# Optimization experiments

Hardware: AMD Instinct MI355X
Metric: run time of the kernel (lower is better)

Reference implementation:

```python
import jax, jax.numpy as jnp
import numpy as np

VOX_X, VOX_Y, VOX_Z = 256, 256, 20   # ceil((pc_range[3:]-pc_range[:3]) / 0.4)
OUT_H, OUT_W, OUT_Z = 200, 200, 16   # hard-coded F.interpolate target in forward
C = 80                               # out_channels; sparse feat dim must match for concat
N_PTS = 200000
BS = 1
EPS = 1e-5


def _lin_interp(x, axis, out_size):
    """1D linear interp along `axis`, matching torch align_corners=False."""
    in_size = x.shape[axis]
    pos = (jnp.arange(out_size, dtype=jnp.float32) + 0.5) * (in_size / out_size) - 0.5
    pos = jnp.clip(pos, 0.0, in_size - 1)
    i0 = jnp.floor(pos).astype(jnp.int32)
    i1 = jnp.minimum(i0 + 1, in_size - 1)
    w = pos - i0.astype(jnp.float32)
    x0 = jnp.take(x, i0, axis=axis)
    x1 = jnp.take(x, i1, axis=axis)
    wshape = [1] * x.ndim
    wshape[axis] = out_size
    w = w.reshape(wshape)
    return x0 * (1.0 - w) + x1 * w


def setup_inputs() -> dict:
    key = jax.random.key(0)
    ks = jax.random.split(key, 8)
    bev_feats = jax.random.normal(ks[0], (BS, C, OUT_H, OUT_W, OUT_Z), dtype=jnp.float32)
    # coords: [batch_idx, x, y, z] with per-column valid ranges
    cb = jax.random.randint(ks[1], (N_PTS, 1), 0, BS, dtype=jnp.int32)
    cx = jax.random.randint(ks[2], (N_PTS, 1), 0, VOX_X, dtype=jnp.int32)
    cy = jax.random.randint(ks[3], (N_PTS, 1), 0, VOX_Y, dtype=jnp.int32)
    cz = jax.random.randint(ks[4], (N_PTS, 1), 0, VOX_Z, dtype=jnp.int32)
    coords = jnp.concatenate([cb, cx, cy, cz], axis=1)
    feats = jax.random.normal(ks[5], (N_PTS, C), dtype=jnp.float32)
    w_conv = jax.random.normal(ks[6], (C, 2 * C), dtype=jnp.float32) * (1.0 / np.sqrt(2 * C))
    b_conv = jnp.zeros((C,), dtype=jnp.float32)
    return {
        "bev_feats": bev_feats, "coords": coords, "feats": feats,
        "w_conv": w_conv, "b_conv": b_conv,
        "bn_gamma": jnp.ones((C,), jnp.float32), "bn_beta": jnp.zeros((C,), jnp.float32),
        "bn_mean": jnp.zeros((C,), jnp.float32), "bn_var": jnp.ones((C,), jnp.float32),
    }


def reference(bev_feats, coords, feats, w_conv, b_conv, bn_gamma, bn_beta, bn_mean, bn_var):
    bs = bev_feats.shape[0]
    voxel = jnp.zeros((bs, VOX_X, VOX_Y, VOX_Z, C), dtype=jnp.float32)
    voxel = voxel.at[coords[:, 0], coords[:, 1], coords[:, 2], coords[:, 3]].set(feats)
    # permute(0,4,2,1,3): (bs, X, Y, Z, C) -> (bs, C, Y, X, Z)
    prior = jnp.transpose(voxel, (0, 4, 2, 1, 3))
    # trilinear interpolate (256,256,20) -> (200,200,16), align_corners=False (separable)
    prior = _lin_interp(prior, 2, OUT_H)
    prior = _lin_interp(prior, 3, OUT_W)
    prior = _lin_interp(prior, 4, OUT_Z)
    # concat on channels -> 1x1x1 conv3d -> BN (eval stats) -> residual -> ReLU
    x = jnp.concatenate([bev_feats, prior], axis=1)  # (bs, 2C, H, W, Z)
    y = jnp.einsum('bchwz,oc->bohwz', x, w_conv) + b_conv[None, :, None, None, None]
    inv = bn_gamma * jax.lax.rsqrt(bn_var + EPS)
    y = y * inv[None, :, None, None, None] + (bn_beta - bn_mean * inv)[None, :, None, None, None]
    return jax.nn.relu(y + bev_feats)
```

## Files before the change

### kernel.cpp

```cpp
#include <hip/hip_runtime.h>
#include <hip/hip_bf16.h>

#define VXX 256
#define VYY 256
#define VZZ 20
#define NC  80
#define OH  200
#define OW  200
#define OZ  16
#define SPATIAL (OH*OW*OZ)
#define NVOX (VXX*VYY*VZZ)
#define EPSV 1e-5f
#define NS 64
#define RS 168
#define NWG (SPATIAL/NS)
#define X_FOOT 6
#define NCELL (2*X_FOOT*VZZ)
#define SLOTS 48
#define STR32 41

typedef float  f32x4 __attribute__((ext_vector_type(4)));
typedef short  s16x8 __attribute__((ext_vector_type(8)));

__device__ __forceinline__ ushort f2bf(float f) {
    uint u = __builtin_bit_cast(uint, f);
    u += 0x7FFFu + ((u >> 16) & 1u);
    return (ushort)(u >> 16);
}

__global__ void init_winner_k(int* __restrict__ w) {
    int i = blockIdx.x * 256 + threadIdx.x;
    if (i < NVOX) w[i] = -1;
}

__global__ void scatter_k(const int* __restrict__ coords, int npts,
                          int* __restrict__ winner) {
    int i = blockIdx.x * 256 + threadIdx.x;
    if (i >= npts) return;
    int b = coords[i*4+0];
    int x = coords[i*4+1];
    int y = coords[i*4+2];
    int z = coords[i*4+3];
    int vi = ((b*VXX + x)*VYY + y)*VZZ + z;
    atomicMax(&winner[vi], i);
}

__global__ void prep_k(const float* __restrict__ wconv,
                       const float* __restrict__ bconv,
                       const float* __restrict__ gamma,
                       const float* __restrict__ beta,
                       const float* __restrict__ mean,
                       const float* __restrict__ var,
                       ushort* __restrict__ wfrag,
                       float2* __restrict__ bnss) {
    int tid = threadIdx.x;
    for (int idx = tid; idx < 25*512; idx += 256) {
        int f   = idx >> 9;
        int rem = idx & 511;
        int l   = rem >> 3;
        int j   = rem & 7;
        int mt  = f / 5;
        int ks  = f - mt*5;
        int o   = mt*16 + (l & 15);
        int c   = ks*32 + (l >> 4)*8 + j;
        wfrag[idx] = f2bf(wconv[o*160 + c]);
    }
    if (tid < NC) {
        float inv = gamma[tid] * rsqrtf(var[tid] + EPSV);
        bnss[tid] = make_float2(inv, bconv[tid]*inv + beta[tid] - mean[tid]*inv);
    }
}

__launch_bounds__(256, 5)
__global__ void fused_k(const float* __restrict__ bev,
                        const float* __restrict__ feats,
                        const int*  __restrict__ winner,
                        const ushort* __restrict__ wfrag,
                        const float2* __restrict__ bnss,
                        float* __restrict__ out) {
    __shared__ __align__(16) ushort x_lds[NS * RS];
    __shared__ uint   rows_lds[SLOTS*STR32];
    __shared__ int    idx_lds[NCELL];
    __shared__ int    slot_pi[SLOTS];
    __shared__ int    wavecnt[4];

    const int tid   = threadIdx.x;
    const int bid   = blockIdx.x;
    const int swzb  = (bid & 7) * (NWG/8) + (bid >> 3);
    const int sbase = swzb * NS;
    const int sl    = tid & 63;
    const int quarter = tid >> 6;
    const int wv    = tid >> 6, lane = tid & 63;

    const int h  = sbase / (OW * OZ);
    const int w0 = (sbase >> 4) % OW;
    float posy = (h + 0.5f) * ((float)VYY/(float)OH) - 0.5f;
    posy = fminf(fmaxf(posy, 0.f), (float)(VYY-1));
    const int   y0 = (int)posy;
    const int   y1 = min(y0+1, VYY-1);
    const float fy = posy - (float)y0;
    float posx0 = (w0 + 0.5f) * ((float)VXX/(float)OW) - 0.5f;
    posx0 = fminf(fmaxf(posx0, 0.f), (float)(VXX-1));
    const int xmin = (int)posx0;

    float4 bv[5];
    {
        const int q16 = lane & 15, mm = lane >> 4;
        #pragma unroll
        for (int it = 0; it < 5; ++it) {
            int cbase = (it*4 + wv) * 4;
            bv[it] = *(const float4*)&bev[(cbase+mm)*SPATIAL + sbase + q16*4];
        }
    }

    int pi = -1;
    if (tid < NCELL) {
        int fz  = tid % VZZ;
        int fx  = (tid / VZZ) % X_FOOT;
        int fyc = tid / (VZZ * X_FOOT);
        int xx  = min(xmin + fx, VXX-1);
        int yy  = fyc ? y1 : y0;
        pi = winner[(xx*VYY + yy)*VZZ + fz];
    }
    unsigned long long bm = __ballot(pi >= 0);
    if (lane == 0) wavecnt[wv] = __popcll(bm);
    __syncthreads();
    int base = 0, nstot = 0;
    #pragma unroll
    for (int w2 = 0; w2 < 4; ++w2) {
        int c2 = wavecnt[w2];
        if (w2 < wv) base += c2;
        nstot += c2;
    }
    if (tid < NCELL) {
        int v = -1;
        if (pi >= 0) {
            int slot = base + __popcll(bm & ((1ull << lane) - 1ull));
            if (slot < SLOTS) { slot_pi[slot] = pi; v = slot; }
            else v = -(pi + 2);
        }
        idx_lds[tid] = v;
    }
    __syncthreads();
    const int nst = min(nstot, SLOTS);

    const float4* feats4 = (const float4*)feats;
    const int myslot = tid >> 2, part = tid & 3;
    const bool rowact = (myslot < nst);
    float4 rbuf[5];
    if (rowact) {
        const float4* p = feats4 + slot_pi[myslot]*20 + part*5;
        #pragma unroll
        for (int q = 0; q < 5; ++q) rbuf[q] = p[q];
    }

    {
        const int q16 = lane & 15, mm = lane >> 4;
        #pragma unroll
        for (int it = 0; it < 5; ++it) {
            int cbase = (it*4 + wv) * 4;
            const float4 v = bv[it];
            uint u0 = (uint)f2bf(v.x) | ((uint)f2bf(v.y) << 16);
            uint u1 = (uint)f2bf(v.z) | ((uint)f2bf(v.w) << 16);
            uint us[4];
            #pragma unroll
            for (int j = 0; j < 4; ++j) {
                int src = q16 + 16*j;
                uint t0 = (uint)__shfl((int)u0, src, 64);
                uint t1 = (uint)__shfl((int)u1, src, 64);
                uint sel = (mm & 2) ? t1 : t0;
                us[j] = (mm & 1) ? (sel >> 16) : (sel & 0xffffu);
            }
            uint2 o2 = make_uint2(us[0] | (us[1] << 16), us[2] | (us[3] << 16));
            int row = q16*4 + mm;
            *(uint2*)&x_lds[row*RS + cbase] = o2;
        }
    }

    if (rowact) {
        uint* dst = &rows_lds[myslot*STR32 + part*10];
        #pragma unroll
        for (int q = 0; q < 5; ++q) {
            dst[2*q]   = (uint)f2bf(rbuf[q].x) | ((uint)f2bf(rbuf[q].y) << 16);
            dst[2*q+1] = (uint)f2bf(rbuf[q].z) | ((uint)f2bf(rbuf[q].w) << 16);
        }
    }
    __syncthreads();

    {
        const int z = sl & 15;
        const int w = w0 + (sl >> 4);
        float posx = (w + 0.5f) * ((float)VXX/(float)OW) - 0.5f;
        posx = fminf(fmaxf(posx, 0.f), (float)(VXX-1));
        int x0 = (int)posx; int x1 = min(x0+1, VXX-1);
        float fxw = posx - (float)x0;
        float posz = (z + 0.5f) * ((float)VZZ/(float)OZ) - 0.5f;
        posz = fminf(fmaxf(posz, 0.f), (float)(VZZ-1));
        int z0 = (int)posz; int z1 = min(z0+1, VZZ-1);
        float fzw = posz - (float)z0;
        const int fx0 = x0 - xmin, fx1 = x1 - xmin;

        float acc20[20];
        #pragma unroll
        for (int j = 0; j < 20; ++j) acc20[j] = 0.f;

        #pragma unroll
        for (int k = 0; k < 8; ++k) {
            int kz = k & 1, kx = (k>>1)&1, ky = k>>2;
            int cell = (ky*X_FOOT + (kx ? fx1 : fx0))*VZZ + (kz ? z1 : z0);
            int v = idx_lds[cell];
            if (v == -1) continue;
            float wtk = (ky?fy:1.f-fy) * (kx?fxw:1.f-fxw) * (kz?fzw:1.f-fzw);
            if (v >= 0) {
                const uint* r = &rows_lds[v*STR32 + quarter*10];
                #pragma unroll
                for (int qq = 0; qq < 10; ++qq) {
                    uint u = r[qq];
                    float lo = __builtin_bit_cast(float, u << 16);
                    float hi = __builtin_bit_cast(float, u & 0xffff0000u);
                    acc20[2*qq]   += wtk * lo;
                    acc20[2*qq+1] += wtk * hi;
                }
            } else {
                const float4* p = feats4 + (-v - 2)*20 + quarter*5;
                #pragma unroll
                for (int q = 0; q < 5; ++q) {
                    float4 f = p[q];
                    acc20[4*q]   += wtk*f.x; acc20[4*q+1] += wtk*f.y;
                    acc20[4*q+2] += wtk*f.z; acc20[4*q+3] += wtk*f.w;
                }
            }
        }

        #pragma unroll
        for (int q = 0; q < 5; ++q) {
            ushort4 pk = make_ushort4(f2bf(acc20[4*q]),   f2bf(acc20[4*q+1]),
                                      f2bf(acc20[4*q+2]), f2bf(acc20[4*q+3]));
            *(ushort4*)&x_lds[sl*RS + 80 + quarter*20 + q*4] = pk;
        }
    }
    __syncthreads();

    const int lrow = lane & 15, lgrp = lane >> 4;

    f32x4 acc[5];
    #pragma unroll
    for (int mt = 0; mt < 5; ++mt) acc[mt] = (f32x4){0.f, 0.f, 0.f, 0.f};

    const int srow = (wv*16 + lrow) * RS;

    #pragma unroll
    for (int ks = 0; ks < 5; ++ks) {
        s16x8 b = *(const s16x8*)&x_lds[srow + ks*32 + lgrp*8];
        #pragma unroll
        for (int mt = 0; mt < 5; ++mt) {
            s16x8 a = *(const s16x8*)&wfrag[((mt*5 + ks)*64 + lane)*8];
            acc[mt] = __builtin_amdgcn_mfma_f32_16x16x32_bf16(a, b, acc[mt], 0, 0, 0);
        }
    }

    const int slocal = wv*16 + lrow;
    const int sglob  = sbase + slocal;
    #pragma unroll
    for (int mt = 0; mt < 5; ++mt) {
        #pragma unroll
        for (int r = 0; r < 4; ++r) {
            int o = mt*16 + lgrp*4 + r;
            float2 ss = bnss[o];
            float resid = __builtin_bit_cast(float, (uint)x_lds[slocal*RS + o] << 16);
            float v = acc[mt][r]*ss.x + ss.y + resid;
            out[o*SPATIAL + sglob] = fmaxf(v, 0.f);
        }
    }
}

extern "C" void kernel_launch(void* const* d_in, const int* in_sizes, int n_in,
                              void* d_out, int out_size, void* d_ws, size_t ws_size,
                              hipStream_t stream) {
    const float* bev    = (const float*)d_in[0];
    const int*   coords = (const int*)  d_in[1];
    const float* feats  = (const float*)d_in[2];
    const float* wconv  = (const float*)d_in[3];
    const float* bconv  = (const float*)d_in[4];
    const float* gamma  = (const float*)d_in[5];
    const float* beta   = (const float*)d_in[6];
    const float* mean   = (const float*)d_in[7];
    const float* var    = (const float*)d_in[8];
    float*       out    = (float*)d_out;

    int*    winner = (int*)d_ws;
    ushort* wfrag  = (ushort*)((char*)d_ws + (size_t)NVOX*4);
    float2* bnss   = (float2*)((char*)d_ws + (size_t)NVOX*4 + 25600);
    int npts = in_sizes[1] / 4;

    hipLaunchKernelGGL(init_winner_k, dim3((NVOX + 255)/256), dim3(256), 0, stream, winner);
    hipLaunchKernelGGL(scatter_k, dim3((npts + 255)/256), dim3(256), 0, stream,
                       coords, npts, winner);
    hipLaunchKernelGGL(prep_k, dim3(1), dim3(256), 0, stream,
                       wconv, bconv, gamma, beta, mean, var, wfrag, bnss);
    hipLaunchKernelGGL(fused_k, dim3(NWG), dim3(256), 0, stream,
                       bev, feats, winner, wfrag, bnss, out);
}
```

Measured before the change: 170.1 us.

## Merge init/prep kernels, load bev per-spatial, use lgkm-only barriers

Fuses the winner-init and weight-prep kernels into one setup kernel, which writes the winner array with int4 stores and removes one launch. In the fused kernel the bev loads become scalar per-thread loads indexed by spatial position, replacing the float4 loads plus shuffle transpose. Those loads are placed between scheduling barriers so they overlap the winner lookups. __syncthreads is replaced with an lgkmcnt-only wait plus s_barrier so outstanding global loads are not drained at each barrier. The residual reads are vectorized into one ushort4 LDS load per tile. Scalar bev loads are coalesced across lanes but issue more instructions and hold more registers.

```diff
diff --git a/kernel.cpp b/kernel.cpp
--- a/kernel.cpp
+++ b/kernel.cpp
@@ -28,9 +28,10 @@
     return (ushort)(u >> 16);
 }
 
-__global__ void init_winner_k(int* __restrict__ w) {
-    int i = blockIdx.x * 256 + threadIdx.x;
-    if (i < NVOX) w[i] = -1;
+__device__ __forceinline__ void bar_lgkm() {
+    asm volatile("s_waitcnt lgkmcnt(0)" ::: "memory");
+    __builtin_amdgcn_s_barrier();
+    asm volatile("" ::: "memory");
 }
 
 __global__ void scatter_k(const int* __restrict__ coords, int npts,
@@ -45,16 +46,20 @@
     atomicMax(&winner[vi], i);
 }
 
-__global__ void prep_k(const float* __restrict__ wconv,
-                       const float* __restrict__ bconv,
-                       const float* __restrict__ gamma,
-                       const float* __restrict__ beta,
-                       const float* __restrict__ mean,
-                       const float* __restrict__ var,
-                       ushort* __restrict__ wfrag,
-                       float2* __restrict__ bnss) {
-    int tid = threadIdx.x;
-    for (int idx = tid; idx < 25*512; idx += 256) {
+__global__ void setup_k(const float* __restrict__ wconv,
+                        const float* __restrict__ bconv,
+                        const float* __restrict__ gamma,
+                        const float* __restrict__ beta,
+                        const float* __restrict__ mean,
+                        const float* __restrict__ var,
+                        int4* __restrict__ winner4,
+                        ushort* __restrict__ wfrag,
+                        float2* __restrict__ bnss) {
+    const int b = blockIdx.x, tid = threadIdx.x;
+    if (b < 1280) {
+        winner4[b*256 + tid] = make_int4(-1, -1, -1, -1);
+    } else if (b < 1330) {
+        int idx = (b - 1280)*256 + tid;
         int f   = idx >> 9;
         int rem = idx & 511;
         int l   = rem >> 3;
@@ -64,8 +69,7 @@
         int o   = mt*16 + (l & 15);
         int c   = ks*32 + (l >> 4)*8 + j;
         wfrag[idx] = f2bf(wconv[o*160 + c]);
-    }
-    if (tid < NC) {
+    } else if (tid < NC) {
         float inv = gamma[tid] * rsqrtf(var[tid] + EPSV);
         bnss[tid] = make_float2(inv, bconv[tid]*inv + beta[tid] - mean[tid]*inv);
     }
@@ -90,7 +94,7 @@
     const int sbase = swzb * NS;
     const int sl    = tid & 63;
     const int quarter = tid >> 6;
-    const int wv    = tid >> 6, lane = tid & 63;
+    const int wv    = quarter, lane = sl;
 
     const int h  = sbase / (OW * OZ);
     const int w0 = (sbase >> 4) % OW;
@@ -103,16 +107,6 @@
     posx0 = fminf(fmaxf(posx0, 0.f), (float)(VXX-1));
     const int xmin = (int)posx0;
 
-    float4 bv[5];
-    {
-        const int q16 = lane & 15, mm = lane >> 4;
-        #pragma unroll
-        for (int it = 0; it < 5; ++it) {
-            int cbase = (it*4 + wv) * 4;
-            bv[it] = *(const float4*)&bev[(cbase+mm)*SPATIAL + sbase + q16*4];
-        }
-    }
-
     int pi = -1;
     if (tid < NCELL) {
         int fz  = tid % VZZ;
@@ -122,9 +116,18 @@
         int yy  = fyc ? y1 : y0;
         pi = winner[(xx*VYY + yy)*VZZ + fz];
     }
+    __builtin_amdgcn_sched_barrier(0);
+
+    const int S = sbase + sl;
+    float bvv[20];
+    #pragma unroll
+    for (int j = 0; j < 20; ++j)
+        bvv[j] = bev[(quarter*20 + j)*SPATIAL + S];
+    __builtin_amdgcn_sched_barrier(0);
+
     unsigned long long bm = __ballot(pi >= 0);
     if (lane == 0) wavecnt[wv] = __popcll(bm);
-    __syncthreads();
+    bar_lgkm();
     int base = 0, nstot = 0;
     #pragma unroll
     for (int w2 = 0; w2 < 4; ++w2) {
@@ -141,7 +144,7 @@
         }
         idx_lds[tid] = v;
     }
-    __syncthreads();
+    bar_lgkm();
     const int nst = min(nstot, SLOTS);
 
     const float4* feats4 = (const float4*)feats;
@@ -154,27 +157,11 @@
         for (int q = 0; q < 5; ++q) rbuf[q] = p[q];
     }
 
-    {
-        const int q16 = lane & 15, mm = lane >> 4;
-        #pragma unroll
-        for (int it = 0; it < 5; ++it) {
-            int cbase = (it*4 + wv) * 4;
-            const float4 v = bv[it];
-            uint u0 = (uint)f2bf(v.x) | ((uint)f2bf(v.y) << 16);
-            uint u1 = (uint)f2bf(v.z) | ((uint)f2bf(v.w) << 16);
-            uint us[4];
-            #pragma unroll
-            for (int j = 0; j < 4; ++j) {
-                int src = q16 + 16*j;
-                uint t0 = (uint)__shfl((int)u0, src, 64);
-                uint t1 = (uint)__shfl((int)u1, src, 64);
-                uint sel = (mm & 2) ? t1 : t0;
-                us[j] = (mm & 1) ? (sel >> 16) : (sel & 0xffffu);
-            }
-            uint2 o2 = make_uint2(us[0] | (us[1] << 16), us[2] | (us[3] << 16));
-            int row = q16*4 + mm;
-            *(uint2*)&x_lds[row*RS + cbase] = o2;
-        }
+    #pragma unroll
+    for (int j5 = 0; j5 < 5; ++j5) {
+        ushort4 pk = make_ushort4(f2bf(bvv[j5*4+0]), f2bf(bvv[j5*4+1]),
+                                  f2bf(bvv[j5*4+2]), f2bf(bvv[j5*4+3]));
+        *(ushort4*)&x_lds[sl*RS + quarter*20 + j5*4] = pk;
     }
 
     if (rowact) {
@@ -185,7 +172,7 @@
             dst[2*q+1] = (uint)f2bf(rbuf[q].z) | ((uint)f2bf(rbuf[q].w) << 16);
         }
     }
-    __syncthreads();
+    bar_lgkm();
 
     {
         const int z = sl & 15;
@@ -239,7 +226,7 @@
             *(ushort4*)&x_lds[sl*RS + 80 + quarter*20 + q*4] = pk;
         }
     }
-    __syncthreads();
+    bar_lgkm();
 
     const int lrow = lane & 15, lgrp = lane >> 4;
 
@@ -263,11 +250,13 @@
     const int sglob  = sbase + slocal;
     #pragma unroll
     for (int mt = 0; mt < 5; ++mt) {
+        ushort4 rr = *(const ushort4*)&x_lds[slocal*RS + mt*16 + lgrp*4];
+        const ushort rrv[4] = {rr.x, rr.y, rr.z, rr.w};
         #pragma unroll
         for (int r = 0; r < 4; ++r) {
             int o = mt*16 + lgrp*4 + r;
             float2 ss = bnss[o];
-            float resid = __builtin_bit_cast(float, (uint)x_lds[slocal*RS + o] << 16);
+            float resid = __builtin_bit_cast(float, (uint)rrv[r] << 16);
             float v = acc[mt][r]*ss.x + ss.y + resid;
             out[o*SPATIAL + sglob] = fmaxf(v, 0.f);
         }
@@ -293,11 +282,11 @@
     float2* bnss   = (float2*)((char*)d_ws + (size_t)NVOX*4 + 25600);
     int npts = in_sizes[1] / 4;
 
-    hipLaunchKernelGGL(init_winner_k, dim3((NVOX + 255)/256), dim3(256), 0, stream, winner);
+    hipLaunchKernelGGL(setup_k, dim3(1331), dim3(256), 0, stream,
+                       wconv, bconv, gamma, beta, mean, var,
+                       (int4*)winner, wfrag, bnss);
     hipLaunchKernelGGL(scatter_k, dim3((npts + 255)/256), dim3(256), 0, stream,
                        coords, npts, winner);
-    hipLaunchKernelGGL(prep_k, dim3(1), dim3(256), 0, stream,
-                       wconv, bconv, gamma, beta, mean, var, wfrag, bnss);
     hipLaunchKernelGGL(fused_k, dim3(NWG), dim3(256), 0, stream,
                        bev, feats, winner, wfrag, bnss, out);
 }
```

Result: faster. 153.2 us (-9.9%).
